# Kernel tuning notes

Measured on AMD Instinct MI355X. Metric: run time of the kernel, lower is better.

The kernel has to match this reference:

```python
import jax, jax.numpy as jnp
import numpy as np

SIZE = 4096
DOWN = SIZE // 16  # reduction_factor = 16 -> 256
N_TASKS = 16
BATCH = 2048
INIT_STD = 0.01


def setup_inputs() -> dict:
    key = jax.random.key(0)
    k_x, k_t, k_wd, k_wu = jax.random.split(key, 4)
    x = jax.random.normal(k_x, (BATCH, SIZE), dtype=jnp.float32)
    task_id = jax.random.randint(k_t, (BATCH,), 0, N_TASKS)
    # Stacked per-task adapter params (init: normal(std=0.01) weights, zero bias)
    Wd = jax.random.normal(k_wd, (N_TASKS, SIZE, DOWN), dtype=jnp.float32) * INIT_STD
    bd = jnp.zeros((N_TASKS, DOWN), dtype=jnp.float32)
    Wu = jax.random.normal(k_wu, (N_TASKS, DOWN, SIZE), dtype=jnp.float32) * INIT_STD
    bu = jnp.zeros((N_TASKS, SIZE), dtype=jnp.float32)
    return {"x": x, "task_id": task_id, "Wd": Wd, "bd": bd, "Wu": Wu, "bu": bu}


def reference(x, task_id, Wd, bd, Wu, bu):
    # Down-projection for all tasks, then select each sample's routed task.
    # [B, T, DOWN] is small (B*T*256), cheaper than gathering [B, SIZE, DOWN] weights.
    down_all = jnp.einsum('bd,tdh->bth', x, Wd) + bd[None]
    down = jnp.take_along_axis(down_all, task_id[:, None, None], axis=1)[:, 0]  # [B, DOWN]
    act = jax.nn.silu(down)
    # Up-projection for all tasks, select routed task. [B, T, SIZE]
    up_all = jnp.einsum('bh,thd->btd', act, Wu) + bu[None]
    up = jnp.take_along_axis(up_all, task_id[:, None, None], axis=1)[:, 0]  # [B, SIZE]
    return x + up  # residual=True (default)
```

## Files before the change

kernel.cpp:

```cpp
#include <hip/hip_runtime.h>
#include <stdint.h>

#define BATCH 2048
#define SIZE 4096
#define DOWN 256
#define NTASK 16
#define KC 16
#define KCHUNK (SIZE / KC)
#define XPAD 128
#define ACTT_N (BATCH + XPAD)

typedef _Float16 half8 __attribute__((ext_vector_type(8)));
typedef float floatx4 __attribute__((ext_vector_type(4)));

__device__ __forceinline__ void async_cp16(void* lds, const void* g) {
    __builtin_amdgcn_global_load_lds((const __attribute__((address_space(1))) uint32_t*)g,
                                     (__attribute__((address_space(3))) uint32_t*)lds, 16, 0, 0);
}

__global__ __launch_bounds__(256) void sort_kernel(const int* __restrict__ task_id,
                                                   int* __restrict__ taskOff,
                                                   int* __restrict__ sortedIdx,
                                                   int* __restrict__ taskOfPos) {
    __shared__ int cnt[NTASK];
    __shared__ int base[NTASK + 1];
    __shared__ int cur[NTASK];
    int tid = threadIdx.x;
    if (tid < NTASK) cnt[tid] = 0;
    __syncthreads();
    for (int i = tid; i < BATCH; i += 256) atomicAdd(&cnt[task_id[i]], 1);
    __syncthreads();
    if (tid == 0) {
        int s = 0;
        for (int t = 0; t < NTASK; t++) { base[t] = s; s += cnt[t]; }
        base[NTASK] = s;
    }
    __syncthreads();
    if (tid < NTASK) { cur[tid] = base[tid]; taskOff[tid] = base[tid]; }
    if (tid == 0) taskOff[NTASK] = BATCH;
    __syncthreads();
    for (int i = tid; i < BATCH; i += 256) {
        int t = task_id[i];
        int p = atomicAdd(&cur[t], 1);
        sortedIdx[p] = i;
        taskOfPos[p] = t;
    }
}

__global__ __launch_bounds__(256) void cvt_x_kernel(const float* __restrict__ x,
                                                    const int* __restrict__ sortedIdx,
                                                    _Float16* __restrict__ x16) {
    int idx = blockIdx.x * 256 + threadIdx.x;
    int pos = idx >> 9, col = (idx & 511) * 8;
    const float* src = x + (size_t)sortedIdx[pos] * SIZE + col;
    float4 f0 = *(const float4*)src;
    float4 f1 = *(const float4*)(src + 4);
    half8 h;
    h[0] = (_Float16)f0.x; h[1] = (_Float16)f0.y; h[2] = (_Float16)f0.z; h[3] = (_Float16)f0.w;
    h[4] = (_Float16)f1.x; h[5] = (_Float16)f1.y; h[6] = (_Float16)f1.z; h[7] = (_Float16)f1.w;
    *(half8*)(x16 + (size_t)pos * SIZE + col) = h;
}

__global__ __launch_bounds__(256) void cvt_w_kernel(const float* __restrict__ Wd,
                                                    const float* __restrict__ Wu,
                                                    half8* __restrict__ Wd16,
                                                    half8* __restrict__ Wu16) {
    int b = blockIdx.x, tid = threadIdx.x;
    if (b < 8192) {
        int idx = b * 256 + tid;
        int n = idx & 255, kg = (idx >> 8) & 511, t = idx >> 17;
        const float* s = Wd + ((size_t)t * SIZE + kg * 8) * DOWN + n;
        half8 h;
#pragma unroll
        for (int e = 0; e < 8; e++) h[e] = (_Float16)s[(size_t)e * DOWN];
        Wd16[idx] = h;
    } else {
        int idx = (b - 8192) * 256 + tid;
        int n = idx & 4095, kg = (idx >> 12) & 31, t = idx >> 17;
        const float* s = Wu + ((size_t)t * DOWN + kg * 8) * SIZE + n;
        half8 h;
#pragma unroll
        for (int e = 0; e < 8; e++) h[e] = (_Float16)s[(size_t)e * SIZE];
        Wu16[idx] = h;
    }
}

__global__ __launch_bounds__(256, 4) void gemm1_kernel(const _Float16* __restrict__ x16,
                                                       const half8* __restrict__ Wd16,
                                                       const int* __restrict__ taskOff,
                                                       _Float16* __restrict__ partial) {
    int task = blockIdx.x, kc = blockIdx.y, nt = blockIdx.z;
    int rowStart = taskOff[task];
    int nrows = taskOff[task + 1] - rowStart;
    if (nrows <= 0) return;

    __shared__ half8 A_lds[8][128];
    __shared__ half8 B_lds[8][128];

    int tid = threadIdx.x;
    int wave = tid >> 6, lane = tid & 63, quad = lane >> 4, l15 = lane & 15;
    int wm = wave >> 1, wn = wave & 1;
    int rowA = tid >> 1, j2 = tid & 1;

    for (int r0 = 0; r0 < nrows; r0 += 128) {
        floatx4 acc[4][4];
#pragma unroll
        for (int mi = 0; mi < 4; mi++)
#pragma unroll
            for (int ni = 0; ni < 4; ni++) acc[mi][ni] = (floatx4){0.f, 0.f, 0.f, 0.f};

        const _Float16* arow = x16 + (size_t)(rowStart + r0 + rowA) * SIZE;

#pragma unroll
        for (int ph = 0; ph < 4; ph++) {
            int k0 = kc * KCHUNK + ph * 64;
            __syncthreads();
            {
                const _Float16* s = arow + k0 + j2 * 32;
                half8 h0 = *(const half8*)(s);
                half8 h1 = *(const half8*)(s + 8);
                half8 h2 = *(const half8*)(s + 16);
                half8 h3 = *(const half8*)(s + 24);
                A_lds[j2 * 4 + 0][rowA] = h0;
                A_lds[j2 * 4 + 1][rowA] = h1;
                A_lds[j2 * 4 + 2][rowA] = h2;
                A_lds[j2 * 4 + 3][rowA] = h3;
            }
            {
                int kgbase = task * 512 + (k0 >> 3);
#pragma unroll
                for (int jj = 0; jj < 2; jj++) {
                    int j = wave * 2 + jj;
#pragma unroll
                    for (int c = 0; c < 2; c++)
                        async_cp16(&B_lds[j][c * 64],
                                   Wd16 + (size_t)(kgbase + j) * 256 + nt * 128 + c * 64 + lane);
                }
            }
            __syncthreads();
#pragma unroll
            for (int ks = 0; ks < 2; ks++) {
                int kg = ks * 4 + quad;
                half8 a[4], b[4];
#pragma unroll
                for (int i = 0; i < 4; i++) a[i] = A_lds[kg][wm * 64 + i * 16 + l15];
#pragma unroll
                for (int i = 0; i < 4; i++) b[i] = B_lds[kg][wn * 64 + i * 16 + l15];
#pragma unroll
                for (int mi = 0; mi < 4; mi++)
#pragma unroll
                    for (int ni = 0; ni < 4; ni++)
                        acc[mi][ni] = __builtin_amdgcn_mfma_f32_16x16x32_f16(
                            a[mi], b[ni], acc[mi][ni], 0, 0, 0);
            }
        }
#pragma unroll
        for (int mi = 0; mi < 4; mi++) {
#pragma unroll
            for (int reg = 0; reg < 4; reg++) {
                int r = r0 + wm * 64 + mi * 16 + quad * 4 + reg;
                if (r < nrows) {
                    size_t off = ((size_t)kc * BATCH + (rowStart + r)) * DOWN + nt * 128;
#pragma unroll
                    for (int ni = 0; ni < 4; ni++)
                        partial[off + wn * 64 + ni * 16 + l15] = (_Float16)acc[mi][ni][reg];
                }
            }
        }
    }
}

__global__ __launch_bounds__(256) void silu_kernel(const half8* __restrict__ partial8,
                                                   const float* __restrict__ bd,
                                                   const int* __restrict__ taskOfPos,
                                                   half8* __restrict__ actT) {
    int idx = blockIdx.x * 256 + threadIdx.x;
    int s = idx >> 5, hg = idx & 31;
    const float* bdr = bd + taskOfPos[s] * DOWN + hg * 8;
    float v[8];
#pragma unroll
    for (int e = 0; e < 8; e++) v[e] = bdr[e];
#pragma unroll
    for (int kc = 0; kc < KC; kc++) {
        half8 p = partial8[((size_t)kc * BATCH + s) * 32 + hg];
#pragma unroll
        for (int e = 0; e < 8; e++) v[e] += (float)p[e];
    }
    half8 h;
#pragma unroll
    for (int e = 0; e < 8; e++) {
        float sv = v[e] / (1.0f + __expf(-v[e]));
        h[e] = (_Float16)sv;
    }
    actT[(size_t)hg * ACTT_N + s] = h;
}

__global__ __launch_bounds__(256, 4) void gemm2_kernel(const half8* __restrict__ actT,
                                                       const half8* __restrict__ Wu16,
                                                       const float* __restrict__ bu,
                                                       const float* __restrict__ x,
                                                       const int* __restrict__ taskOff,
                                                       const int* __restrict__ sortedIdx,
                                                       float* __restrict__ out) {
    int task = blockIdx.x, nt = blockIdx.y;
    int rowStart = taskOff[task];
    int nrows = taskOff[task + 1] - rowStart;
    if (nrows <= 0) return;

    __shared__ half8 A_lds[8][128];
    __shared__ half8 B_lds[8][128];

    int tid = threadIdx.x;
    int wave = tid >> 6, lane = tid & 63, quad = lane >> 4, l15 = lane & 15;
    int wm = wave >> 1, wn = wave & 1;
    int ncol0 = nt * 128;

    for (int r0 = 0; r0 < nrows; r0 += 128) {
        floatx4 acc[4][4];
#pragma unroll
        for (int mi = 0; mi < 4; mi++)
#pragma unroll
            for (int ni = 0; ni < 4; ni++) acc[mi][ni] = (floatx4){0.f, 0.f, 0.f, 0.f};

#pragma unroll
        for (int ph = 0; ph < 4; ph++) {
            int kgbase = ph * 8;
            __syncthreads();
#pragma unroll
            for (int jj = 0; jj < 2; jj++) {
                int j = wave * 2 + jj;
#pragma unroll
                for (int c = 0; c < 2; c++) {
                    async_cp16(&A_lds[j][c * 64],
                               actT + (size_t)(kgbase + j) * ACTT_N + rowStart + r0 + c * 64 + lane);
                    async_cp16(&B_lds[j][c * 64],
                               Wu16 + (size_t)(task * 32 + kgbase + j) * SIZE + ncol0 + c * 64 + lane);
                }
            }
            __syncthreads();
#pragma unroll
            for (int ks = 0; ks < 2; ks++) {
                int kg = ks * 4 + quad;
                half8 a[4], b[4];
#pragma unroll
                for (int i = 0; i < 4; i++) a[i] = A_lds[kg][wm * 64 + i * 16 + l15];
#pragma unroll
                for (int i = 0; i < 4; i++) b[i] = B_lds[kg][wn * 64 + i * 16 + l15];
#pragma unroll
                for (int mi = 0; mi < 4; mi++)
#pragma unroll
                    for (int ni = 0; ni < 4; ni++)
                        acc[mi][ni] = __builtin_amdgcn_mfma_f32_16x16x32_f16(
                            a[mi], b[ni], acc[mi][ni], 0, 0, 0);
            }
        }
#pragma unroll
        for (int mi = 0; mi < 4; mi++) {
#pragma unroll
            for (int reg = 0; reg < 4; reg++) {
                int r = r0 + wm * 64 + mi * 16 + quad * 4 + reg;
                if (r < nrows) {
                    int b = sortedIdx[rowStart + r];
                    const float* xr = x + (size_t)b * SIZE;
                    float* outr = out + (size_t)b * SIZE;
#pragma unroll
                    for (int ni = 0; ni < 4; ni++) {
                        int n = ncol0 + wn * 64 + ni * 16 + l15;
                        outr[n] = acc[mi][ni][reg] + bu[task * SIZE + n] + xr[n];
                    }
                }
            }
        }
    }
}

extern "C" void kernel_launch(void* const* d_in, const int* in_sizes, int n_in,
                              void* d_out, int out_size, void* d_ws, size_t ws_size,
                              hipStream_t stream) {
    const float* x       = (const float*)d_in[0];
    const int*   task_id = (const int*)d_in[1];
    const float* Wd      = (const float*)d_in[2];
    const float* bd      = (const float*)d_in[3];
    const float* Wu      = (const float*)d_in[4];
    const float* bu      = (const float*)d_in[5];
    float* out = (float*)d_out;

    _Float16* partial = (_Float16*)d_out;

    char* ws = (char*)d_ws;
    _Float16* x16 = (_Float16*)ws;            ws += (size_t)(BATCH + XPAD) * SIZE * 2;
    half8* Wd16   = (half8*)ws;               ws += (size_t)NTASK * 512 * 256 * 16;
    half8* Wu16   = (half8*)ws;               ws += (size_t)NTASK * 32 * 4096 * 16;
    half8* actT   = (half8*)ws;               ws += (size_t)32 * ACTT_N * 16;
    int* taskOff   = (int*)ws;
    int* sortedIdx = taskOff + 32;
    int* taskOfPos = sortedIdx + BATCH;

    sort_kernel<<<1, 256, 0, stream>>>(task_id, taskOff, sortedIdx, taskOfPos);
    cvt_x_kernel<<<(BATCH * 512) / 256, 256, 0, stream>>>(x, sortedIdx, x16);
    cvt_w_kernel<<<16384, 256, 0, stream>>>(Wd, Wu, Wd16, Wu16);
    gemm1_kernel<<<dim3(NTASK, KC, 2), 256, 0, stream>>>(x16, Wd16, taskOff, partial);
    silu_kernel<<<(BATCH * 32) / 256, 256, 0, stream>>>((const half8*)partial, bd, taskOfPos, actT);
    gemm2_kernel<<<dim3(NTASK, SIZE / 128), 256, 0, stream>>>(actT, Wu16, bu, x, taskOff,
                                                              sortedIdx, out);
}
```

Before: 285.3 us.

## Fuse fp32-to-fp16 conversion of x and weights into GEMM tile loads

Removes the separate x and weight conversion kernels and their fp16 workspace copies. gemm1 now gathers fp32 x rows through sortedIdx and converts them while staging into LDS. Both GEMMs async-copy fp32 weight rows into padded LDS and convert to fp16 when building MFMA fragments. This removes an extra read-write pass over the large weight tensors. The K split in gemm1 doubles so more blocks run. In exchange the code issues many 4-byte async loads and does strided scalar LDS reads plus conversions in the inner loop.

```diff
diff --git a/kernel.cpp b/kernel.cpp
--- a/kernel.cpp
+++ b/kernel.cpp
@@ -5,17 +5,24 @@
 #define SIZE 4096
 #define DOWN 256
 #define NTASK 16
-#define KC 16
+#define KC 32
 #define KCHUNK (SIZE / KC)
 #define XPAD 128
 #define ACTT_N (BATCH + XPAD)
+#define BPITCH 130
 
 typedef _Float16 half8 __attribute__((ext_vector_type(8)));
 typedef float floatx4 __attribute__((ext_vector_type(4)));
+
+__device__ __forceinline__ int imin(int a, int b) { return a < b ? a : b; }
 
 __device__ __forceinline__ void async_cp16(void* lds, const void* g) {
     __builtin_amdgcn_global_load_lds((const __attribute__((address_space(1))) uint32_t*)g,
                                      (__attribute__((address_space(3))) uint32_t*)lds, 16, 0, 0);
+}
+__device__ __forceinline__ void async_cp4(void* lds, const void* g) {
+    __builtin_amdgcn_global_load_lds((const __attribute__((address_space(1))) uint32_t*)g,
+                                     (__attribute__((address_space(3))) uint32_t*)lds, 4, 0, 0);
 }
 
 __global__ __launch_bounds__(256) void sort_kernel(const int* __restrict__ task_id,
@@ -47,60 +54,24 @@
     }
 }
 
-__global__ __launch_bounds__(256) void cvt_x_kernel(const float* __restrict__ x,
+__global__ __launch_bounds__(256) void gemm1_kernel(const float* __restrict__ x,
+                                                    const float* __restrict__ Wd,
+                                                    const int* __restrict__ taskOff,
                                                     const int* __restrict__ sortedIdx,
-                                                    _Float16* __restrict__ x16) {
-    int idx = blockIdx.x * 256 + threadIdx.x;
-    int pos = idx >> 9, col = (idx & 511) * 8;
-    const float* src = x + (size_t)sortedIdx[pos] * SIZE + col;
-    float4 f0 = *(const float4*)src;
-    float4 f1 = *(const float4*)(src + 4);
-    half8 h;
-    h[0] = (_Float16)f0.x; h[1] = (_Float16)f0.y; h[2] = (_Float16)f0.z; h[3] = (_Float16)f0.w;
-    h[4] = (_Float16)f1.x; h[5] = (_Float16)f1.y; h[6] = (_Float16)f1.z; h[7] = (_Float16)f1.w;
-    *(half8*)(x16 + (size_t)pos * SIZE + col) = h;
-}
-
-__global__ __launch_bounds__(256) void cvt_w_kernel(const float* __restrict__ Wd,
-                                                    const float* __restrict__ Wu,
-                                                    half8* __restrict__ Wd16,
-                                                    half8* __restrict__ Wu16) {
-    int b = blockIdx.x, tid = threadIdx.x;
-    if (b < 8192) {
-        int idx = b * 256 + tid;
-        int n = idx & 255, kg = (idx >> 8) & 511, t = idx >> 17;
-        const float* s = Wd + ((size_t)t * SIZE + kg * 8) * DOWN + n;
-        half8 h;
-#pragma unroll
-        for (int e = 0; e < 8; e++) h[e] = (_Float16)s[(size_t)e * DOWN];
-        Wd16[idx] = h;
-    } else {
-        int idx = (b - 8192) * 256 + tid;
-        int n = idx & 4095, kg = (idx >> 12) & 31, t = idx >> 17;
-        const float* s = Wu + ((size_t)t * DOWN + kg * 8) * SIZE + n;
-        half8 h;
-#pragma unroll
-        for (int e = 0; e < 8; e++) h[e] = (_Float16)s[(size_t)e * SIZE];
-        Wu16[idx] = h;
-    }
-}
-
-__global__ __launch_bounds__(256, 4) void gemm1_kernel(const _Float16* __restrict__ x16,
-                                                       const half8* __restrict__ Wd16,
-                                                       const int* __restrict__ taskOff,
-                                                       _Float16* __restrict__ partial) {
+                                                    _Float16* __restrict__ partial) {
     int task = blockIdx.x, kc = blockIdx.y, nt = blockIdx.z;
     int rowStart = taskOff[task];
     int nrows = taskOff[task + 1] - rowStart;
     if (nrows <= 0) return;
 
-    __shared__ half8 A_lds[8][128];
-    __shared__ half8 B_lds[8][128];
+    __shared__ float B_ldsf[32 * BPITCH];
+    __shared__ half8 A_lds[4][128];
 
     int tid = threadIdx.x;
     int wave = tid >> 6, lane = tid & 63, quad = lane >> 4, l15 = lane & 15;
     int wm = wave >> 1, wn = wave & 1;
     int rowA = tid >> 1, j2 = tid & 1;
+    const float* Wdt = Wd + (size_t)task * SIZE * DOWN;
 
     for (int r0 = 0; r0 < nrows; r0 += 128) {
         floatx4 acc[4][4];
@@ -109,50 +80,55 @@
 #pragma unroll
             for (int ni = 0; ni < 4; ni++) acc[mi][ni] = (floatx4){0.f, 0.f, 0.f, 0.f};
 
-        const _Float16* arow = x16 + (size_t)(rowStart + r0 + rowA) * SIZE;
+        int asrc = sortedIdx[rowStart + imin(r0 + rowA, nrows - 1)];
+        const float* xrow = x + (size_t)asrc * SIZE;
 
 #pragma unroll
         for (int ph = 0; ph < 4; ph++) {
-            int k0 = kc * KCHUNK + ph * 64;
+            int kglob = kc * KCHUNK + ph * 32;
             __syncthreads();
             {
-                const _Float16* s = arow + k0 + j2 * 32;
-                half8 h0 = *(const half8*)(s);
-                half8 h1 = *(const half8*)(s + 8);
-                half8 h2 = *(const half8*)(s + 16);
-                half8 h3 = *(const half8*)(s + 24);
-                A_lds[j2 * 4 + 0][rowA] = h0;
-                A_lds[j2 * 4 + 1][rowA] = h1;
-                A_lds[j2 * 4 + 2][rowA] = h2;
-                A_lds[j2 * 4 + 3][rowA] = h3;
-            }
-            {
-                int kgbase = task * 512 + (k0 >> 3);
-#pragma unroll
-                for (int jj = 0; jj < 2; jj++) {
-                    int j = wave * 2 + jj;
-#pragma unroll
-                    for (int c = 0; c < 2; c++)
-                        async_cp16(&B_lds[j][c * 64],
-                                   Wd16 + (size_t)(kgbase + j) * 256 + nt * 128 + c * 64 + lane);
-                }
-            }
-            __syncthreads();
-#pragma unroll
-            for (int ks = 0; ks < 2; ks++) {
-                int kg = ks * 4 + quad;
-                half8 a[4], b[4];
-#pragma unroll
-                for (int i = 0; i < 4; i++) a[i] = A_lds[kg][wm * 64 + i * 16 + l15];
-#pragma unroll
-                for (int i = 0; i < 4; i++) b[i] = B_lds[kg][wn * 64 + i * 16 + l15];
-#pragma unroll
-                for (int mi = 0; mi < 4; mi++)
-#pragma unroll
-                    for (int ni = 0; ni < 4; ni++)
-                        acc[mi][ni] = __builtin_amdgcn_mfma_f32_16x16x32_f16(
-                            a[mi], b[ni], acc[mi][ni], 0, 0, 0);
-            }
+                const float* s = xrow + kglob + j2 * 16;
+                float4 f0 = *(const float4*)(s);
+                float4 f1 = *(const float4*)(s + 4);
+                float4 f2 = *(const float4*)(s + 8);
+                float4 f3 = *(const float4*)(s + 12);
+                half8 h0, h1;
+                h0[0] = (_Float16)f0.x; h0[1] = (_Float16)f0.y;
+                h0[2] = (_Float16)f0.z; h0[3] = (_Float16)f0.w;
+                h0[4] = (_Float16)f1.x; h0[5] = (_Float16)f1.y;
+                h0[6] = (_Float16)f1.z; h0[7] = (_Float16)f1.w;
+                h1[0] = (_Float16)f2.x; h1[1] = (_Float16)f2.y;
+                h1[2] = (_Float16)f2.z; h1[3] = (_Float16)f2.w;
+                h1[4] = (_Float16)f3.x; h1[5] = (_Float16)f3.y;
+                h1[6] = (_Float16)f3.z; h1[7] = (_Float16)f3.w;
+                A_lds[j2 * 2 + 0][rowA] = h0;
+                A_lds[j2 * 2 + 1][rowA] = h1;
+            }
+#pragma unroll
+            for (int rr = 0; rr < 8; rr++) {
+                int r = wave * 8 + rr;
+                const float* src = Wdt + (size_t)(kglob + r) * DOWN + nt * 128 + lane;
+                async_cp4(&B_ldsf[r * BPITCH], src);
+                async_cp4(&B_ldsf[r * BPITCH + 64], src + 64);
+            }
+            __syncthreads();
+            half8 a[4], b[4];
+#pragma unroll
+            for (int i = 0; i < 4; i++) a[i] = A_lds[quad][wm * 64 + i * 16 + l15];
+#pragma unroll
+            for (int i = 0; i < 4; i++) {
+                int n = wn * 64 + i * 16 + l15;
+                const float* bp = &B_ldsf[quad * 8 * BPITCH + n];
+#pragma unroll
+                for (int j = 0; j < 8; j++) b[i][j] = (_Float16)bp[j * BPITCH];
+            }
+#pragma unroll
+            for (int mi = 0; mi < 4; mi++)
+#pragma unroll
+                for (int ni = 0; ni < 4; ni++)
+                    acc[mi][ni] = __builtin_amdgcn_mfma_f32_16x16x32_f16(
+                        a[mi], b[ni], acc[mi][ni], 0, 0, 0);
         }
 #pragma unroll
         for (int mi = 0; mi < 4; mi++) {
@@ -195,25 +171,26 @@
     actT[(size_t)hg * ACTT_N + s] = h;
 }
 
-__global__ __launch_bounds__(256, 4) void gemm2_kernel(const half8* __restrict__ actT,
-                                                       const half8* __restrict__ Wu16,
-                                                       const float* __restrict__ bu,
-                                                       const float* __restrict__ x,
-                                                       const int* __restrict__ taskOff,
-                                                       const int* __restrict__ sortedIdx,
-                                                       float* __restrict__ out) {
+__global__ __launch_bounds__(256) void gemm2_kernel(const half8* __restrict__ actT,
+                                                    const float* __restrict__ Wu,
+                                                    const float* __restrict__ bu,
+                                                    const float* __restrict__ x,
+                                                    const int* __restrict__ taskOff,
+                                                    const int* __restrict__ sortedIdx,
+                                                    float* __restrict__ out) {
     int task = blockIdx.x, nt = blockIdx.y;
     int rowStart = taskOff[task];
     int nrows = taskOff[task + 1] - rowStart;
     if (nrows <= 0) return;
 
+    __shared__ float B_ldsf[64 * BPITCH];
     __shared__ half8 A_lds[8][128];
-    __shared__ half8 B_lds[8][128];
 
     int tid = threadIdx.x;
     int wave = tid >> 6, lane = tid & 63, quad = lane >> 4, l15 = lane & 15;
     int wm = wave >> 1, wn = wave & 1;
     int ncol0 = nt * 128;
+    const float* Wut = Wu + (size_t)task * DOWN * SIZE;
 
     for (int r0 = 0; r0 < nrows; r0 += 128) {
         floatx4 acc[4][4];
@@ -224,28 +201,36 @@
 
 #pragma unroll
         for (int ph = 0; ph < 4; ph++) {
-            int kgbase = ph * 8;
+            int kb = ph * 64;
             __syncthreads();
 #pragma unroll
             for (int jj = 0; jj < 2; jj++) {
                 int j = wave * 2 + jj;
-#pragma unroll
-                for (int c = 0; c < 2; c++) {
-                    async_cp16(&A_lds[j][c * 64],
-                               actT + (size_t)(kgbase + j) * ACTT_N + rowStart + r0 + c * 64 + lane);
-                    async_cp16(&B_lds[j][c * 64],
-                               Wu16 + (size_t)(task * 32 + kgbase + j) * SIZE + ncol0 + c * 64 + lane);
+                const half8* src = actT + (size_t)(ph * 8 + j) * ACTT_N + rowStart + r0 + lane;
+                async_cp16(&A_lds[j][0], src);
+                async_cp16(&A_lds[j][64], src + 64);
+            }
+#pragma unroll
+            for (int rr = 0; rr < 16; rr++) {
+                int r = wave * 16 + rr;
+                const float* src = Wut + (size_t)(kb + r) * SIZE + ncol0 + lane;
+                async_cp4(&B_ldsf[r * BPITCH], src);
+                async_cp4(&B_ldsf[r * BPITCH + 64], src + 64);
+            }
+            __syncthreads();
+#pragma unroll
+            for (int ks = 0; ks < 2; ks++) {
+                half8 a[4], b[4];
+#pragma unroll
+                for (int i = 0; i < 4; i++)
+                    a[i] = A_lds[ks * 4 + quad][wm * 64 + i * 16 + l15];
+#pragma unroll
+                for (int i = 0; i < 4; i++) {
+                    int n = wn * 64 + i * 16 + l15;
+                    const float* bp = &B_ldsf[(ks * 32 + quad * 8) * BPITCH + n];
+#pragma unroll
+                    for (int j = 0; j < 8; j++) b[i][j] = (_Float16)bp[j * BPITCH];
                 }
-            }
-            __syncthreads();
-#pragma unroll
-            for (int ks = 0; ks < 2; ks++) {
-                int kg = ks * 4 + quad;
-                half8 a[4], b[4];
-#pragma unroll
-                for (int i = 0; i < 4; i++) a[i] = A_lds[kg][wm * 64 + i * 16 + l15];
-#pragma unroll
-                for (int i = 0; i < 4; i++) b[i] = B_lds[kg][wn * 64 + i * 16 + l15];
 #pragma unroll
                 for (int mi = 0; mi < 4; mi++)
 #pragma unroll
@@ -288,19 +273,14 @@
     _Float16* partial = (_Float16*)d_out;
 
     char* ws = (char*)d_ws;
-    _Float16* x16 = (_Float16*)ws;            ws += (size_t)(BATCH + XPAD) * SIZE * 2;
-    half8* Wd16   = (half8*)ws;               ws += (size_t)NTASK * 512 * 256 * 16;
-    half8* Wu16   = (half8*)ws;               ws += (size_t)NTASK * 32 * 4096 * 16;
-    half8* actT   = (half8*)ws;               ws += (size_t)32 * ACTT_N * 16;
+    half8* actT = (half8*)ws;                 ws += (size_t)32 * ACTT_N * 16;
     int* taskOff   = (int*)ws;
     int* sortedIdx = taskOff + 32;
     int* taskOfPos = sortedIdx + BATCH;
 
     sort_kernel<<<1, 256, 0, stream>>>(task_id, taskOff, sortedIdx, taskOfPos);
-    cvt_x_kernel<<<(BATCH * 512) / 256, 256, 0, stream>>>(x, sortedIdx, x16);
-    cvt_w_kernel<<<16384, 256, 0, stream>>>(Wd, Wu, Wd16, Wu16);
-    gemm1_kernel<<<dim3(NTASK, KC, 2), 256, 0, stream>>>(x16, Wd16, taskOff, partial);
+    gemm1_kernel<<<dim3(NTASK, KC, 2), 256, 0, stream>>>(x, Wd, taskOff, sortedIdx, partial);
     silu_kernel<<<(BATCH * 32) / 256, 256, 0, stream>>>((const half8*)partial, bd, taskOfPos, actT);
-    gemm2_kernel<<<dim3(NTASK, SIZE / 128), 256, 0, stream>>>(actT, Wu16, bu, x, taskOff,
-                                                              sortedIdx, out);
-}
+    gemm2_kernel<<<dim3(NTASK, 32), 256, 0, stream>>>(actT, Wu, bu, x, taskOff,
+                                                      sortedIdx, out);
+}
```

Result: slower. 312.9 us (+9.7%).
